# Kernel optimization log

Measured on AMD Instinct MI355X. Metric: run time of the kernel, lower is better.

## Reference

```python
import jax, jax.numpy as jnp
import numpy as np
from jax import lax

B, T, C = 64, 1024, 512
INIT_P = 1.0
CLAMP_LO, CLAMP_HI = 1e-4, 1.0 - 1e-4


def setup_inputs() -> dict:
    key = jax.random.key(0)
    k1, k2 = jax.random.split(key)
    x = jax.random.normal(k1, (B, T, C), dtype=jnp.float32)
    # learnable per-channel logit(lambda); original inits to logit(0.98) repeated,
    # use randn around that value so gradients are nontrivial
    init_logit = float(np.log(0.98 / (1.0 - 0.98)))
    logit_lambda = init_logit + 0.1 * jax.random.normal(k2, (C,), dtype=jnp.float32)
    return {"x": x, "logit_lambda": logit_lambda}


def reference(x, logit_lambda):
    # lam: [C] -> broadcast over (B, C) states
    lam = jnp.clip(jax.nn.sigmoid(logit_lambda), CLAMP_LO, CLAMP_HI)
    theta0 = x[:, 0, :]                                   # [B, C]
    P0 = jnp.full(theta0.shape, INIT_P, dtype=x.dtype)    # [B, C]

    def step(carry, xt):
        theta, P = carry
        K = P / (lam + P)                 # gain, data-independent of x
        theta = theta + K * (xt - theta)  # level update
        P = (P - K * P) / lam             # covariance update
        return (theta, P), theta

    xs = jnp.swapaxes(x, 0, 1)[1:]        # [T-1, B, C], timesteps 1..T-1
    _, ys = lax.scan(step, (theta0, P0), xs)
    # y[:,0,:] = x[:,0,:], y[:,t,:] = theta_t for t>=1
    y = jnp.concatenate([theta0[:, None, :], jnp.swapaxes(ys, 0, 1)], axis=1)
    return y
```

## Files before the change

kernel.cpp:

```cpp
#include <hip/hip_runtime.h>
#include <math.h>


namespace {
constexpr int kB = 64;
constexpr int kT = 1024;
constexpr int kC = 512;
constexpr int kNCH = 32;
constexpr int kL = kT / kNCH;
constexpr int kCV = kC / 4;
constexpr int kChunks = kB * kNCH;
constexpr int kBlocks = kChunks / 2;
constexpr size_t kCarryOffB = 1024;
constexpr size_t kCarryU64 = (size_t)kChunks * kCV * 4;
}

typedef float vfloat4 __attribute__((ext_vector_type(4)));

__device__ __forceinline__ void load_lam(const float* __restrict__ zl, int c0,
                                         float lam[4]) {
  vfloat4 z = *reinterpret_cast<const vfloat4*>(zl + c0);
#pragma unroll
  for (int k = 0; k < 4; ++k) {
    float s = 1.0f / (1.0f + expf(-z[k]));
    lam[k] = fminf(fmaxf(s, 1e-4f), 1.0f - 1e-4f);
  }
}

__device__ __forceinline__ unsigned long long ld_carry(
    const unsigned long long* __restrict__ p) {
  return __hip_atomic_load(p, __ATOMIC_RELAXED, __HIP_MEMORY_SCOPE_AGENT);
}

__device__ __forceinline__ void poll4(const unsigned long long* __restrict__ p,
                                      float v[4]) {
  unsigned long long u0 = ld_carry(p + 0);
  unsigned long long u1 = ld_carry(p + 1);
  unsigned long long u2 = ld_carry(p + 2);
  unsigned long long u3 = ld_carry(p + 3);
  while (!((u0 >> 32) & (u1 >> 32) & (u2 >> 32) & (u3 >> 32))) {
    __builtin_amdgcn_s_sleep(1);
    u0 = ld_carry(p + 0);
    u1 = ld_carry(p + 1);
    u2 = ld_carry(p + 2);
    u3 = ld_carry(p + 3);
  }
  union { unsigned u32; float f; } c;
  c.u32 = (unsigned)u0; v[0] = c.f;
  c.u32 = (unsigned)u1; v[1] = c.f;
  c.u32 = (unsigned)u2; v[2] = c.f;
  c.u32 = (unsigned)u3; v[3] = c.f;
}

extern "C" __global__ __launch_bounds__(256) void ewrls_init(
    unsigned long long* __restrict__ cw, unsigned* __restrict__ tk) {
  size_t i = (size_t)blockIdx.x * 256 + threadIdx.x;
  if (i < kCarryU64) cw[i] = 0ull;
  if (i == 0) *tk = 0u;
}

extern "C" __global__ __launch_bounds__(256) void ewrls_fused(
    const float* __restrict__ x, const float* __restrict__ zl,
    unsigned* __restrict__ ws, float* __restrict__ y) {
  __shared__ unsigned sh_t;
  if (threadIdx.x == 0)
    sh_t = __hip_atomic_fetch_add(ws, 1u, __ATOMIC_RELAXED,
                                  __HIP_MEMORY_SCOPE_AGENT);
  __syncthreads();
  const unsigned T = sh_t;
  const int c = (int)(2u * T) + (int)(threadIdx.x >> 7);
  const int j = c >> 6;
  const int b = c & 63;
  const int cv = threadIdx.x & 127;

  unsigned long long* __restrict__ carry =
      reinterpret_cast<unsigned long long*>(
          reinterpret_cast<char*>(ws) + kCarryOffB);

  float lam[4];
  load_lam(zl, cv * 4, lam);

  const size_t base = ((size_t)b * kT + (size_t)j * kL) * kCV + cv;
  const vfloat4* xp = reinterpret_cast<const vfloat4*>(x) + base;
  float a0 = 0.f, a1 = 0.f, a2 = 0.f, a3 = 0.f;
#pragma unroll 8
  for (int t = 0; t < kL; ++t) {
    vfloat4 v = xp[(size_t)t * kCV];
    a0 = fmaf(lam[0], a0, v.x);
    a1 = fmaf(lam[1], a1, v.y);
    a2 = fmaf(lam[2], a2, v.z);
    a3 = fmaf(lam[3], a3, v.w);
  }

  {
    unsigned long long* cp = carry + (((size_t)c * kCV + cv) << 2);
    union { float f; unsigned u; } q;
    q.f = a0;
    __hip_atomic_store(cp + 0, (1ull << 32) | q.u, __ATOMIC_RELAXED,
                       __HIP_MEMORY_SCOPE_AGENT);
    q.f = a1;
    __hip_atomic_store(cp + 1, (1ull << 32) | q.u, __ATOMIC_RELAXED,
                       __HIP_MEMORY_SCOPE_AGENT);
    q.f = a2;
    __hip_atomic_store(cp + 2, (1ull << 32) | q.u, __ATOMIC_RELAXED,
                       __HIP_MEMORY_SCOPE_AGENT);
    q.f = a3;
    __hip_atomic_store(cp + 3, (1ull << 32) | q.u, __ATOMIC_RELAXED,
                       __HIP_MEMORY_SCOPE_AGENT);
  }

  float lamL[4];
#pragma unroll
  for (int k = 0; k < 4; ++k) {
    float p = lam[k];
#pragma unroll
    for (int q = 0; q < 5; ++q) p = p * p;
    lamL[k] = p;
  }

  float S0 = 0.f, S1 = 0.f, S2 = 0.f, S3 = 0.f;
  float p0 = 1.f, p1 = 1.f, p2 = 1.f, p3 = 1.f;
  for (int i = 0; i < j; ++i) {
    const unsigned long long* cp =
        carry + ((((size_t)i * kB + b) * kCV + cv) << 2);
    float v[4];
    poll4(cp, v);
    S0 = fmaf(lamL[0], S0, v[0]);
    S1 = fmaf(lamL[1], S1, v[1]);
    S2 = fmaf(lamL[2], S2, v[2]);
    S3 = fmaf(lamL[3], S3, v[3]);
    p0 *= lamL[0];
    p1 *= lamL[1];
    p2 *= lamL[2];
    p3 *= lamL[3];
  }

  float Q0 = (1.0f - p0) * __builtin_amdgcn_rcpf(1.0f - lam[0]);
  float Q1 = (1.0f - p1) * __builtin_amdgcn_rcpf(1.0f - lam[1]);
  float Q2 = (1.0f - p2) * __builtin_amdgcn_rcpf(1.0f - lam[2]);
  float Q3 = (1.0f - p3) * __builtin_amdgcn_rcpf(1.0f - lam[3]);

  vfloat4* yp = reinterpret_cast<vfloat4*>(y) + base;
#pragma unroll 8
  for (int t = 0; t < kL; ++t) {
    vfloat4 v = __builtin_nontemporal_load(&xp[(size_t)t * kCV]);
    S0 = fmaf(lam[0], S0, v.x);
    S1 = fmaf(lam[1], S1, v.y);
    S2 = fmaf(lam[2], S2, v.z);
    S3 = fmaf(lam[3], S3, v.w);
    Q0 = fmaf(lam[0], Q0, 1.0f);
    Q1 = fmaf(lam[1], Q1, 1.0f);
    Q2 = fmaf(lam[2], Q2, 1.0f);
    Q3 = fmaf(lam[3], Q3, 1.0f);
    vfloat4 o;
    o.x = S0 * __builtin_amdgcn_rcpf(Q0);
    o.y = S1 * __builtin_amdgcn_rcpf(Q1);
    o.z = S2 * __builtin_amdgcn_rcpf(Q2);
    o.w = S3 * __builtin_amdgcn_rcpf(Q3);
    __builtin_nontemporal_store(o, &yp[(size_t)t * kCV]);
  }
}

extern "C" __global__ __launch_bounds__(256) void ewrls_serial(
    const float* __restrict__ x, const float* __restrict__ zl,
    float* __restrict__ y) {
  int idx = blockIdx.x * 256 + threadIdx.x;
  int cv = idx % kCV;
  int b = idx / kCV;
  float lam[4];
  load_lam(zl, cv * 4, lam);
  float S[4] = {0.f, 0.f, 0.f, 0.f};
  float Q[4] = {0.f, 0.f, 0.f, 0.f};
  const size_t base = (size_t)b * kT * kCV + cv;
  const vfloat4* xp = reinterpret_cast<const vfloat4*>(x) + base;
  vfloat4* yp = reinterpret_cast<vfloat4*>(y) + base;
#pragma unroll 4
  for (int t = 0; t < kT; ++t) {
    vfloat4 v = xp[(size_t)t * kCV];
    S[0] = fmaf(lam[0], S[0], v.x);
    S[1] = fmaf(lam[1], S[1], v.y);
    S[2] = fmaf(lam[2], S[2], v.z);
    S[3] = fmaf(lam[3], S[3], v.w);
    Q[0] = fmaf(lam[0], Q[0], 1.0f);
    Q[1] = fmaf(lam[1], Q[1], 1.0f);
    Q[2] = fmaf(lam[2], Q[2], 1.0f);
    Q[3] = fmaf(lam[3], Q[3], 1.0f);
    vfloat4 o;
    o.x = S[0] * __builtin_amdgcn_rcpf(Q[0]);
    o.y = S[1] * __builtin_amdgcn_rcpf(Q[1]);
    o.z = S[2] * __builtin_amdgcn_rcpf(Q[2]);
    o.w = S[3] * __builtin_amdgcn_rcpf(Q[3]);
    yp[(size_t)t * kCV] = o;
  }
}

extern "C" void kernel_launch(void* const* d_in, const int* in_sizes, int n_in,
                              void* d_out, int out_size, void* d_ws,
                              size_t ws_size, hipStream_t stream) {
  const float* x = (const float*)d_in[0];
  const float* zl = (const float*)d_in[1];
  float* y = (float*)d_out;

  const size_t need = kCarryOffB + kCarryU64 * 8;
  if (ws_size >= need) {
    unsigned* ws = (unsigned*)d_ws;
    unsigned long long* cw = reinterpret_cast<unsigned long long*>(
        reinterpret_cast<char*>(d_ws) + kCarryOffB);
    ewrls_init<<<(int)((kCarryU64 + 255) / 256), 256, 0, stream>>>(cw, ws);
    ewrls_fused<<<kBlocks, 256, 0, stream>>>(x, zl, ws, y);
  } else {
    const int n = kB * kCV;
    ewrls_serial<<<n / 256, 256, 0, stream>>>(x, zl, y);
  }
}
```

Baseline: 289.5 us.

## Use two-level chunked scan with intra-block LDS prefix and fewer global carries

Restructures the decoupled chunked scan so each 512-thread block owns a 128-step window split into four 32-step subchunks. The subchunks combine their local aggregates through LDS, and only subchunk 0 publishes a window carry and polls up to 7 predecessors, instead of each chunk polling up to 31 global carries. This cuts global atomic polling and the serial lookback chain. In exchange it adds two block barriers, uses larger blocks, and leaves threads idle while subchunk 0 waits on predecessors.

```diff
diff --git a/kernel.cpp b/kernel.cpp
--- a/kernel.cpp
+++ b/kernel.cpp
@@ -6,11 +6,12 @@
 constexpr int kB = 64;
 constexpr int kT = 1024;
 constexpr int kC = 512;
-constexpr int kNCH = 32;
-constexpr int kL = kT / kNCH;
+constexpr int kTW = 8;
+constexpr int kWL = kT / kTW;
+constexpr int kSC = 4;
+constexpr int kSL = kWL / kSC;
 constexpr int kCV = kC / 4;
-constexpr int kChunks = kB * kNCH;
-constexpr int kBlocks = kChunks / 2;
+constexpr int kChunks = kB * kTW;
 constexpr size_t kCarryOffB = 1024;
 constexpr size_t kCarryU64 = (size_t)kChunks * kCV * 4;
 }
@@ -59,18 +60,20 @@
   if (i == 0) *tk = 0u;
 }
 
-extern "C" __global__ __launch_bounds__(256) void ewrls_fused(
+extern "C" __global__ __launch_bounds__(512) void ewrls_fused(
     const float* __restrict__ x, const float* __restrict__ zl,
     unsigned* __restrict__ ws, float* __restrict__ y) {
   __shared__ unsigned sh_t;
+  __shared__ vfloat4 lds_agg[kSC][kCV];
+  __shared__ vfloat4 lds_G[kCV];
   if (threadIdx.x == 0)
     sh_t = __hip_atomic_fetch_add(ws, 1u, __ATOMIC_RELAXED,
                                   __HIP_MEMORY_SCOPE_AGENT);
   __syncthreads();
-  const unsigned T = sh_t;
-  const int c = (int)(2u * T) + (int)(threadIdx.x >> 7);
+  const int c = (int)sh_t;
   const int j = c >> 6;
   const int b = c & 63;
+  const int s = threadIdx.x >> 7;
   const int cv = threadIdx.x & 127;
 
   unsigned long long* __restrict__ carry =
@@ -80,69 +83,117 @@
   float lam[4];
   load_lam(zl, cv * 4, lam);
 
-  const size_t base = ((size_t)b * kT + (size_t)j * kL) * kCV + cv;
+  float lam32[4];
+#pragma unroll
+  for (int k = 0; k < 4; ++k) {
+    float p = lam[k];
+#pragma unroll
+    for (int q = 0; q < 5; ++q) p = p * p;
+    lam32[k] = p;
+  }
+
+  const size_t base =
+      ((size_t)b * kT + (size_t)j * kWL + (size_t)s * kSL) * kCV + cv;
   const vfloat4* xp = reinterpret_cast<const vfloat4*>(x) + base;
   float a0 = 0.f, a1 = 0.f, a2 = 0.f, a3 = 0.f;
 #pragma unroll 8
-  for (int t = 0; t < kL; ++t) {
+  for (int t = 0; t < kSL; ++t) {
     vfloat4 v = xp[(size_t)t * kCV];
     a0 = fmaf(lam[0], a0, v.x);
     a1 = fmaf(lam[1], a1, v.y);
     a2 = fmaf(lam[2], a2, v.z);
     a3 = fmaf(lam[3], a3, v.w);
   }
-
   {
-    unsigned long long* cp = carry + (((size_t)c * kCV + cv) << 2);
-    union { float f; unsigned u; } q;
-    q.f = a0;
-    __hip_atomic_store(cp + 0, (1ull << 32) | q.u, __ATOMIC_RELAXED,
-                       __HIP_MEMORY_SCOPE_AGENT);
-    q.f = a1;
-    __hip_atomic_store(cp + 1, (1ull << 32) | q.u, __ATOMIC_RELAXED,
-                       __HIP_MEMORY_SCOPE_AGENT);
-    q.f = a2;
-    __hip_atomic_store(cp + 2, (1ull << 32) | q.u, __ATOMIC_RELAXED,
-                       __HIP_MEMORY_SCOPE_AGENT);
-    q.f = a3;
-    __hip_atomic_store(cp + 3, (1ull << 32) | q.u, __ATOMIC_RELAXED,
-                       __HIP_MEMORY_SCOPE_AGENT);
-  }
-
-  float lamL[4];
+    vfloat4 a = {a0, a1, a2, a3};
+    lds_agg[s][cv] = a;
+  }
+  __syncthreads();
+
+  float S0 = 0.f, S1 = 0.f, S2 = 0.f, S3 = 0.f;
+  for (int i = 0; i < s; ++i) {
+    vfloat4 ai = lds_agg[i][cv];
+    S0 = fmaf(lam32[0], S0, ai.x);
+    S1 = fmaf(lam32[1], S1, ai.y);
+    S2 = fmaf(lam32[2], S2, ai.z);
+    S3 = fmaf(lam32[3], S3, ai.w);
+  }
+
+  float l128[4];
 #pragma unroll
   for (int k = 0; k < 4; ++k) {
-    float p = lam[k];
-#pragma unroll
-    for (int q = 0; q < 5; ++q) p = p * p;
-    lamL[k] = p;
-  }
-
-  float S0 = 0.f, S1 = 0.f, S2 = 0.f, S3 = 0.f;
-  float p0 = 1.f, p1 = 1.f, p2 = 1.f, p3 = 1.f;
+    float p = lam32[k];
+    p = p * p;
+    l128[k] = p * p;
+  }
+
+  if (s == 0) {
+    float A0 = 0.f, A1 = 0.f, A2 = 0.f, A3 = 0.f;
+#pragma unroll
+    for (int i = 0; i < kSC; ++i) {
+      vfloat4 ai = lds_agg[i][cv];
+      A0 = fmaf(lam32[0], A0, ai.x);
+      A1 = fmaf(lam32[1], A1, ai.y);
+      A2 = fmaf(lam32[2], A2, ai.z);
+      A3 = fmaf(lam32[3], A3, ai.w);
+    }
+    {
+      unsigned long long* cp = carry + (((size_t)c * kCV + cv) << 2);
+      union { float f; unsigned u; } q;
+      q.f = A0;
+      __hip_atomic_store(cp + 0, (1ull << 32) | q.u, __ATOMIC_RELAXED,
+                         __HIP_MEMORY_SCOPE_AGENT);
+      q.f = A1;
+      __hip_atomic_store(cp + 1, (1ull << 32) | q.u, __ATOMIC_RELAXED,
+                         __HIP_MEMORY_SCOPE_AGENT);
+      q.f = A2;
+      __hip_atomic_store(cp + 2, (1ull << 32) | q.u, __ATOMIC_RELAXED,
+                         __HIP_MEMORY_SCOPE_AGENT);
+      q.f = A3;
+      __hip_atomic_store(cp + 3, (1ull << 32) | q.u, __ATOMIC_RELAXED,
+                         __HIP_MEMORY_SCOPE_AGENT);
+    }
+    float G0 = 0.f, G1 = 0.f, G2 = 0.f, G3 = 0.f;
+    for (int i = 0; i < j; ++i) {
+      const unsigned long long* cp =
+          carry + ((((size_t)i * kB + b) * kCV + cv) << 2);
+      float v[4];
+      poll4(cp, v);
+      G0 = fmaf(l128[0], G0, v[0]);
+      G1 = fmaf(l128[1], G1, v[1]);
+      G2 = fmaf(l128[2], G2, v[2]);
+      G3 = fmaf(l128[3], G3, v[3]);
+    }
+    vfloat4 g = {G0, G1, G2, G3};
+    lds_G[cv] = g;
+  }
+  __syncthreads();
+
+  float sc[4] = {1.f, 1.f, 1.f, 1.f};
+  for (int i = 0; i < s; ++i) {
+#pragma unroll
+    for (int k = 0; k < 4; ++k) sc[k] *= lam32[k];
+  }
+  float pj[4] = {1.f, 1.f, 1.f, 1.f};
   for (int i = 0; i < j; ++i) {
-    const unsigned long long* cp =
-        carry + ((((size_t)i * kB + b) * kCV + cv) << 2);
-    float v[4];
-    poll4(cp, v);
-    S0 = fmaf(lamL[0], S0, v[0]);
-    S1 = fmaf(lamL[1], S1, v[1]);
-    S2 = fmaf(lamL[2], S2, v[2]);
-    S3 = fmaf(lamL[3], S3, v[3]);
-    p0 *= lamL[0];
-    p1 *= lamL[1];
-    p2 *= lamL[2];
-    p3 *= lamL[3];
-  }
-
-  float Q0 = (1.0f - p0) * __builtin_amdgcn_rcpf(1.0f - lam[0]);
-  float Q1 = (1.0f - p1) * __builtin_amdgcn_rcpf(1.0f - lam[1]);
-  float Q2 = (1.0f - p2) * __builtin_amdgcn_rcpf(1.0f - lam[2]);
-  float Q3 = (1.0f - p3) * __builtin_amdgcn_rcpf(1.0f - lam[3]);
+#pragma unroll
+    for (int k = 0; k < 4; ++k) pj[k] *= l128[k];
+  }
+  {
+    vfloat4 g = lds_G[cv];
+    S0 = fmaf(sc[0], g.x, S0);
+    S1 = fmaf(sc[1], g.y, S1);
+    S2 = fmaf(sc[2], g.z, S2);
+    S3 = fmaf(sc[3], g.w, S3);
+  }
+  float Q0 = (1.0f - pj[0] * sc[0]) * __builtin_amdgcn_rcpf(1.0f - lam[0]);
+  float Q1 = (1.0f - pj[1] * sc[1]) * __builtin_amdgcn_rcpf(1.0f - lam[1]);
+  float Q2 = (1.0f - pj[2] * sc[2]) * __builtin_amdgcn_rcpf(1.0f - lam[2]);
+  float Q3 = (1.0f - pj[3] * sc[3]) * __builtin_amdgcn_rcpf(1.0f - lam[3]);
 
   vfloat4* yp = reinterpret_cast<vfloat4*>(y) + base;
 #pragma unroll 8
-  for (int t = 0; t < kL; ++t) {
+  for (int t = 0; t < kSL; ++t) {
     vfloat4 v = __builtin_nontemporal_load(&xp[(size_t)t * kCV]);
     S0 = fmaf(lam[0], S0, v.x);
     S1 = fmaf(lam[1], S1, v.y);
@@ -207,7 +258,7 @@
     unsigned long long* cw = reinterpret_cast<unsigned long long*>(
         reinterpret_cast<char*>(d_ws) + kCarryOffB);
     ewrls_init<<<(int)((kCarryU64 + 255) / 256), 256, 0, stream>>>(cw, ws);
-    ewrls_fused<<<kBlocks, 256, 0, stream>>>(x, zl, ws, y);
+    ewrls_fused<<<kChunks, 512, 0, stream>>>(x, zl, ws, y);
   } else {
     const int n = kB * kCV;
     ewrls_serial<<<n / 256, 256, 0, stream>>>(x, zl, y);
```

After: 254.3 us. 12.2% less time.
